# Optimization experiments

Measured on AMD Instinct MI355X. Metric: run time of the kernel, lower is better.

Reference implementation:

```python
import jax, jax.numpy as jnp
import numpy as np


def setup_inputs() -> dict:
    key = jax.random.key(0)
    ks = jax.random.split(key, 9)
    B, S, D = 4, 1024, 1024
    std = 0.02
    return {
        "x": jax.random.normal(ks[0], (B, S, D), dtype=jnp.float32),
        "W_q": jax.random.normal(ks[1], (D, D), dtype=jnp.float32) * std,
        "b_q": jnp.zeros((D,), dtype=jnp.float32),
        "W_k": jax.random.normal(ks[2], (D, D), dtype=jnp.float32) * std,
        "b_k": jnp.zeros((D,), dtype=jnp.float32),
        "W_v": jax.random.normal(ks[3], (D, D), dtype=jnp.float32) * std,
        "b_v": jnp.zeros((D,), dtype=jnp.float32),
        "W_o": jax.random.normal(ks[4], (D, D), dtype=jnp.float32) * std,
        "b_o": jnp.zeros((D,), dtype=jnp.float32),
        "n_heads": 16,
    }


def reference(x, W_q, b_q, W_k, b_k, W_v, b_v, W_o, b_o, n_heads):
    # x: [B, S, D]; torch Linear convention: y = x @ W.T + b, W is [out, in]
    B, S, D = x.shape
    d_k = D // n_heads
    scale = 1.0 / jnp.sqrt(jnp.asarray(d_k, dtype=x.dtype))

    def split_heads(t):  # [B,S,D] -> [B,H,S,d_k]
        return t.reshape(B, S, n_heads, d_k).transpose(0, 2, 1, 3)

    q = split_heads(x @ W_q.T + b_q)
    k = split_heads(x @ W_k.T + b_k)
    v = split_heads(x @ W_v.T + b_v)

    # scores: [B,H,L,S]
    scores = jnp.einsum("bhld,bhsd->bhls", q, k) * scale
    # causal bias (is_casual=True): -inf above the diagonal
    causal = jnp.tril(jnp.ones((S, S), dtype=bool))
    scores = jnp.where(causal[None, None, :, :], scores, jnp.asarray(-jnp.inf, dtype=scores.dtype))
    attn_w = jax.nn.softmax(scores, axis=-1)  # dropout_p = 0.0 -> identity

    y = jnp.einsum("bhls,bhsd->bhld", attn_w, v)  # [B,H,S,d_k]
    y = y.transpose(0, 2, 1, 3).reshape(B, S, D)
    y = y @ W_o.T + b_o  # output dropout p = 0.0 -> identity
    return (attn_w, y)
```

## Files before the change

kernel.cpp:

```cpp
#include <hip/hip_runtime.h>
#include <hip/hip_bf16.h>
#include <stdint.h>


typedef short short8 __attribute__((ext_vector_type(8)));
typedef short short4v __attribute__((ext_vector_type(4)));
typedef float f32x4 __attribute__((ext_vector_type(4)));

__device__ __forceinline__ short f2bf(float f) {
    union { __hip_bfloat16 h; short s; } u;
    u.h = __float2bfloat16(f);
    return u.s;
}
__device__ __forceinline__ float bf2f(short s) {
    union { uint32_t u; float f; } c;
    c.u = ((uint32_t)(uint16_t)s) << 16;
    return c.f;
}

#define GLD16(g, l) __builtin_amdgcn_global_load_lds( \
    (const __attribute__((address_space(1))) void*)(g), \
    (__attribute__((address_space(3))) void*)(l), 16, 0, 0)

__global__ __launch_bounds__(256) void castall_kernel(const float* __restrict__ x,
                                                      const float* __restrict__ w0,
                                                      const float* __restrict__ w1,
                                                      const float* __restrict__ w2,
                                                      const float* __restrict__ w3,
                                                      short* __restrict__ xb,
                                                      short* __restrict__ qkv,
                                                      short* __restrict__ wo) {
    const int seg = blockIdx.y;
    const float* src;
    short* dst;
    if (seg < 4) {
        src = seg == 0 ? w0 : seg == 1 ? w1 : seg == 2 ? w2 : w3;
        dst = seg < 3 ? qkv + (size_t)seg * 1048576 : wo;
    } else {
        src = x + (size_t)(seg - 4) * 1048576;
        dst = xb + (size_t)(seg - 4) * 1048576;
    }
    for (int i = blockIdx.x * 256 + threadIdx.x; i < 262144; i += gridDim.x * 256) {
        float4 v = ((const float4*)src)[i];
        short4v o;
        o[0] = f2bf(v.x); o[1] = f2bf(v.y); o[2] = f2bf(v.z); o[3] = f2bf(v.w);
        ((short4v*)dst)[i] = o;
    }
}

__global__ __launch_bounds__(256) void gemm_bt(const short* __restrict__ A,
                                               const short* __restrict__ Bw,
                                               const float* __restrict__ b0,
                                               const float* __restrict__ b1,
                                               const float* __restrict__ b2,
                                               short* __restrict__ outq,
                                               short* __restrict__ outk,
                                               short* __restrict__ outv,
                                               float* __restrict__ fout,
                                               int mode) {
    __shared__ __align__(16) short As[2][128 * 32];
    __shared__ __align__(16) short Bs[2][128 * 32];

    const int tid = threadIdx.x;
    const int wave = tid >> 6, lane = tid & 63;
    const int l15 = lane & 15, l4 = lane >> 4;
    const int wm = wave >> 1, wn = wave & 1;
    const int tM = blockIdx.y * 128, tN = blockIdx.x * 128;

    f32x4 acc[4][4] = {};

    auto stage = [&](int buf, int kt) {
        #pragma unroll
        for (int rep = 0; rep < 2; ++rep) {
            int slot = (wave * 2 + rep) * 64 + lane;
            int e0 = slot * 8;
            int row = e0 >> 5, col = e0 & 31;
            GLD16(&A[(size_t)(tM + row) * 1024 + kt + col],
                  (char*)&As[buf][0] + (size_t)(wave * 2 + rep) * 1024);
            GLD16(&Bw[(size_t)(tN + row) * 1024 + kt + col],
                  (char*)&Bs[buf][0] + (size_t)(wave * 2 + rep) * 1024);
        }
    };

    stage(0, 0);
    __syncthreads();
    int cur = 0;

    for (int t = 0; t < 32; ++t) {
        if (t < 31) stage(cur ^ 1, (t + 1) * 32);

        short8 af[4], bfr[4];
        #pragma unroll
        for (int f = 0; f < 4; ++f) {
            af[f]  = *(const short8*)&As[cur][(wm * 64 + f * 16 + l15) * 32 + l4 * 8];
            bfr[f] = *(const short8*)&Bs[cur][(wn * 64 + f * 16 + l15) * 32 + l4 * 8];
        }
        #pragma unroll
        for (int i = 0; i < 4; ++i)
            #pragma unroll
            for (int j = 0; j < 4; ++j)
                acc[i][j] = __builtin_amdgcn_mfma_f32_16x16x32_bf16(af[i], bfr[j], acc[i][j], 0, 0, 0);

        __syncthreads();
        cur ^= 1;
    }

    const int seg = tN >> 10;
    const float* bias = (mode == 3) ? b0 : (seg == 0 ? b0 : seg == 1 ? b1 : b2);

    #pragma unroll
    for (int i = 0; i < 4; ++i) {
        #pragma unroll
        for (int j = 0; j < 4; ++j) {
            if (mode == 4 && seg == 2) {
                int gr0 = tM + wm * 64 + i * 16 + l4 * 4;
                int gc  = tN + wn * 64 + j * 16 + l15;
                int nloc = gc & 1023;
                int bb = gr0 >> 10, s0 = gr0 & 1023, h = nloc >> 6, dk = nloc & 63;
                float bv_ = bias[nloc];
                short4v pk;
                #pragma unroll
                for (int v = 0; v < 4; ++v) pk[v] = f2bf(acc[i][j][v] + bv_);
                *(short4v*)&outv[(((size_t)bb * 16 + h) * 64 + dk) * 1024 + s0] = pk;
            } else {
                #pragma unroll
                for (int v = 0; v < 4; ++v) {
                    int gr = tM + wm * 64 + i * 16 + l4 * 4 + v;
                    int gc = tN + wn * 64 + j * 16 + l15;
                    if (mode == 3) {
                        fout[(size_t)gr * 1024 + gc] = acc[i][j][v] + bias[gc];
                    } else {
                        int nloc = gc & 1023;
                        float val = acc[i][j][v] + bias[nloc];
                        int bb = gr >> 10, s = gr & 1023, h = nloc >> 6, dk = nloc & 63;
                        if (seg == 0) {
                            outq[(((size_t)bb * 16 + h) * 1024 + s) * 64 + dk] = f2bf(val * 0.125f);
                        } else {
                            outk[(((size_t)bb * 16 + h) * 1024 + s) * 64 + dk] = f2bf(val);
                        }
                    }
                }
            }
        }
    }
}

__global__ __launch_bounds__(512, 4) void attn_kernel(const short* __restrict__ q,
                                                      const short* __restrict__ k,
                                                      const short* __restrict__ vT,
                                                      float* __restrict__ attn,
                                                      short* __restrict__ yh) {
    const int bh = blockIdx.x;
    const int y = blockIdx.y;
    const int qb = (y & 1) ? (31 - (y >> 1)) : (y >> 1);
    const int tid = threadIdx.x;
    const int wave = tid >> 6, lane = tid & 63;
    const int l15 = lane & 15, l4 = lane >> 4;
    const int rg = wave & 1, cg = wave >> 1;
    const int q0 = qb * 32;
    const int rbase = q0 + rg * 16;
    const int c0w = cg * 256;

    __shared__ __align__(16) short pb[32][1032];
    __shared__ float mred[4][32];
    __shared__ float sred[4][32];

    short8 qf[2];
    {
        const short* qrow = q + ((size_t)bh * 1024 + rbase + l15) * 64;
        qf[0] = *(const short8*)(qrow + l4 * 8);
        qf[1] = *(const short8*)(qrow + 32 + l4 * 8);
    }

    f32x4 sc[16] = {};
    #pragma unroll
    for (int cf = 0; cf < 16; ++cf) {
        if (c0w + cf * 16 < rbase + 16) {
            const short* krow = k + ((size_t)bh * 1024 + c0w + cf * 16 + l15) * 64;
            short8 kf0 = *(const short8*)(krow + l4 * 8);
            short8 kf1 = *(const short8*)(krow + 32 + l4 * 8);
            sc[cf] = __builtin_amdgcn_mfma_f32_16x16x32_bf16(qf[0], kf0, sc[cf], 0, 0, 0);
            sc[cf] = __builtin_amdgcn_mfma_f32_16x16x32_bf16(qf[1], kf1, sc[cf], 0, 0, 0);
        }
    }

    float mrow[4];
    #pragma unroll
    for (int j = 0; j < 4; ++j) {
        int rglob = rbase + l4 * 4 + j;
        float m = -1e30f;
        #pragma unroll
        for (int cf = 0; cf < 16; ++cf) {
            int col = c0w + cf * 16 + l15;
            m = fmaxf(m, (col <= rglob) ? sc[cf][j] : -1e30f);
        }
        m = fmaxf(m, __shfl_xor(m, 1));
        m = fmaxf(m, __shfl_xor(m, 2));
        m = fmaxf(m, __shfl_xor(m, 4));
        m = fmaxf(m, __shfl_xor(m, 8));
        mrow[j] = m;
    }
    if (l15 == 0) {
        #pragma unroll
        for (int j = 0; j < 4; ++j) mred[cg][rg * 16 + l4 * 4 + j] = mrow[j];
    }
    __syncthreads();
    #pragma unroll
    for (int j = 0; j < 4; ++j) {
        int r = rg * 16 + l4 * 4 + j;
        mrow[j] = fmaxf(fmaxf(mred[0][r], mred[1][r]), fmaxf(mred[2][r], mred[3][r]));
    }

    float inv[4], ls[4];
    #pragma unroll
    for (int j = 0; j < 4; ++j) {
        int rglob = rbase + l4 * 4 + j;
        float s = 0.f;
        #pragma unroll
        for (int cf = 0; cf < 16; ++cf) {
            int col = c0w + cf * 16 + l15;
            float e = (col <= rglob) ? __expf(sc[cf][j] - mrow[j]) : 0.f;
            sc[cf][j] = e;
            s += e;
        }
        s += __shfl_xor(s, 1);
        s += __shfl_xor(s, 2);
        s += __shfl_xor(s, 4);
        s += __shfl_xor(s, 8);
        ls[j] = s;
    }
    if (l15 == 0) {
        #pragma unroll
        for (int j = 0; j < 4; ++j) sred[cg][rg * 16 + l4 * 4 + j] = ls[j];
    }
    __syncthreads();
    #pragma unroll
    for (int j = 0; j < 4; ++j) {
        int r = rg * 16 + l4 * 4 + j;
        inv[j] = 1.0f / (sred[0][r] + sred[1][r] + sred[2][r] + sred[3][r]);
    }

    {
        float* abase = attn + (size_t)bh * 1048576;
        #pragma unroll
        for (int cf = 0; cf < 16; ++cf) {
            const bool keep = (c0w + cf * 16 < q0 + 64);
            const int col = c0w + cf * 16 + l15;
            #pragma unroll
            for (int j = 0; j < 4; ++j) {
                const int row = rg * 16 + l4 * 4 + j;
                float p = sc[cf][j] * inv[j];
                __builtin_nontemporal_store(p, &abase[(size_t)(q0 + row) * 1024 + col]);
                if (keep) pb[row][col] = f2bf(p);
            }
        }
    }
    __syncthreads();

    f32x4 yacc = {};
    {
        const short* vrow = vT + ((size_t)bh * 64 + cg * 16 + l15) * 1024;
        const int nch = (rbase + 16 + 31) >> 5;
        for (int ks = 0; ks < nch; ++ks) {
            short8 pf = *(const short8*)&pb[rg * 16 + l15][ks * 32 + l4 * 8];
            short8 vf = *(const short8*)(vrow + ks * 32 + l4 * 8);
            yacc = __builtin_amdgcn_mfma_f32_16x16x32_bf16(pf, vf, yacc, 0, 0, 0);
        }
    }

    const int b = bh >> 4, h = bh & 15;
    #pragma unroll
    for (int j = 0; j < 4; ++j) {
        yh[((size_t)b * 1024 + rbase + l4 * 4 + j) * 1024 + h * 64 + cg * 16 + l15] = f2bf(yacc[j]);
    }
}

extern "C" void kernel_launch(void* const* d_in, const int* in_sizes, int n_in,
                              void* d_out, int out_size, void* d_ws, size_t ws_size,
                              hipStream_t stream) {
    const float* x  = (const float*)d_in[0];
    const float* Wq = (const float*)d_in[1];
    const float* bq = (const float*)d_in[2];
    const float* Wk = (const float*)d_in[3];
    const float* bk = (const float*)d_in[4];
    const float* Wv = (const float*)d_in[5];
    const float* bv = (const float*)d_in[6];
    const float* Wo = (const float*)d_in[7];
    const float* bo = (const float*)d_in[8];

    char* ws = (char*)d_ws;
    short* xb   = (short*)(ws + ((size_t)0 << 20));
    short* wqkv = (short*)(ws + ((size_t)8 << 20));
    short* wob  = (short*)(ws + ((size_t)14 << 20));
    short* qbp  = (short*)(ws + ((size_t)16 << 20));
    short* kbp  = (short*)(ws + ((size_t)24 << 20));
    short* vTb  = (short*)(ws + ((size_t)32 << 20));
    short* yh   = (short*)(ws + ((size_t)40 << 20));

    float* attn = (float*)d_out;
    float* yout = attn + (size_t)67108864;

    castall_kernel<<<dim3(128, 8), 256, 0, stream>>>(x, Wq, Wk, Wv, Wo, xb, wqkv, wob);

    gemm_bt<<<dim3(24, 32), 256, 0, stream>>>(xb, wqkv, bq, bk, bv, qbp, kbp, vTb, nullptr, 4);

    attn_kernel<<<dim3(64, 32), 512, 0, stream>>>(qbp, kbp, vTb, attn, yh);

    gemm_bt<<<dim3(8, 32), 256, 0, stream>>>(yh, wob, bo, bo, bo, nullptr, nullptr, nullptr, yout, 3);
}
```

Baseline: 201.0 us.

## Use 256x256 tiles with block swizzle for the fused QKV projection GEMM

The shared mode-switched GEMM is split into two kernels. The QKV projection now uses 512-thread blocks computing 256x256 tiles (8 row fragments per wave), with a swizzled 1D block index to improve L2 reuse. The output projection keeps the original 128x128 kernel without the mode branches. Larger tiles raise arithmetic intensity per LDS load, but the launch shrinks to 192 blocks, fewer than the CU count, and register pressure grows.

After: 194.9 us. 3.1% less time.

```diff
diff --git a/kernel.cpp b/kernel.cpp
--- a/kernel.cpp
+++ b/kernel.cpp
@@ -48,26 +48,28 @@
     }
 }
 
-__global__ __launch_bounds__(256) void gemm_bt(const short* __restrict__ A,
-                                               const short* __restrict__ Bw,
-                                               const float* __restrict__ b0,
-                                               const float* __restrict__ b1,
-                                               const float* __restrict__ b2,
-                                               short* __restrict__ outq,
-                                               short* __restrict__ outk,
-                                               short* __restrict__ outv,
-                                               float* __restrict__ fout,
-                                               int mode) {
-    __shared__ __align__(16) short As[2][128 * 32];
-    __shared__ __align__(16) short Bs[2][128 * 32];
+__global__ __launch_bounds__(512, 2) void gemm_qkv256(const short* __restrict__ A,
+                                                      const short* __restrict__ Bw,
+                                                      const float* __restrict__ b0,
+                                                      const float* __restrict__ b1,
+                                                      const float* __restrict__ b2,
+                                                      short* __restrict__ outq,
+                                                      short* __restrict__ outk,
+                                                      short* __restrict__ outv) {
+    __shared__ __align__(16) short As[2][256 * 32];
+    __shared__ __align__(16) short Bs[2][256 * 32];
 
     const int tid = threadIdx.x;
     const int wave = tid >> 6, lane = tid & 63;
     const int l15 = lane & 15, l4 = lane >> 4;
-    const int wm = wave >> 1, wn = wave & 1;
-    const int tM = blockIdx.y * 128, tN = blockIdx.x * 128;
-
-    f32x4 acc[4][4] = {};
+    const int wm = wave >> 2, wn = wave & 3;
+
+    const int lin = blockIdx.x;
+    const int swz = (lin & 7) * 24 + (lin >> 3);
+    const int by = swz & 15, bx = swz >> 4;
+    const int tM = by * 256, tN = bx * 256;
+
+    f32x4 acc[8][4] = {};
 
     auto stage = [&](int buf, int kt) {
         #pragma unroll
@@ -89,14 +91,16 @@
     for (int t = 0; t < 32; ++t) {
         if (t < 31) stage(cur ^ 1, (t + 1) * 32);
 
-        short8 af[4], bfr[4];
-        #pragma unroll
-        for (int f = 0; f < 4; ++f) {
-            af[f]  = *(const short8*)&As[cur][(wm * 64 + f * 16 + l15) * 32 + l4 * 8];
+        short8 af[8], bfr[4];
+        #pragma unroll
+        for (int f = 0; f < 8; ++f)
+            af[f] = *(const short8*)&As[cur][(wm * 128 + f * 16 + l15) * 32 + l4 * 8];
+        #pragma unroll
+        for (int f = 0; f < 4; ++f)
             bfr[f] = *(const short8*)&Bs[cur][(wn * 64 + f * 16 + l15) * 32 + l4 * 8];
-        }
-        #pragma unroll
-        for (int i = 0; i < 4; ++i)
+
+        #pragma unroll
+        for (int i = 0; i < 8; ++i)
             #pragma unroll
             for (int j = 0; j < 4; ++j)
                 acc[i][j] = __builtin_amdgcn_mfma_f32_16x16x32_bf16(af[i], bfr[j], acc[i][j], 0, 0, 0);
@@ -106,18 +110,19 @@
     }
 
     const int seg = tN >> 10;
-    const float* bias = (mode == 3) ? b0 : (seg == 0 ? b0 : seg == 1 ? b1 : b2);
-
-    #pragma unroll
-    for (int i = 0; i < 4; ++i) {
+    const float* bias = seg == 0 ? b0 : seg == 1 ? b1 : b2;
+
+    #pragma unroll
+    for (int i = 0; i < 8; ++i) {
         #pragma unroll
         for (int j = 0; j < 4; ++j) {
-            if (mode == 4 && seg == 2) {
-                int gr0 = tM + wm * 64 + i * 16 + l4 * 4;
-                int gc  = tN + wn * 64 + j * 16 + l15;
-                int nloc = gc & 1023;
-                int bb = gr0 >> 10, s0 = gr0 & 1023, h = nloc >> 6, dk = nloc & 63;
-                float bv_ = bias[nloc];
+            int gc = tN + wn * 64 + j * 16 + l15;
+            int nloc = gc & 1023;
+            int h = nloc >> 6, dk = nloc & 63;
+            float bv_ = bias[nloc];
+            if (seg == 2) {
+                int gr0 = tM + wm * 128 + i * 16 + l4 * 4;
+                int bb = gr0 >> 10, s0 = gr0 & 1023;
                 short4v pk;
                 #pragma unroll
                 for (int v = 0; v < 4; ++v) pk[v] = f2bf(acc[i][j][v] + bv_);
@@ -125,21 +130,80 @@
             } else {
                 #pragma unroll
                 for (int v = 0; v < 4; ++v) {
-                    int gr = tM + wm * 64 + i * 16 + l4 * 4 + v;
-                    int gc = tN + wn * 64 + j * 16 + l15;
-                    if (mode == 3) {
-                        fout[(size_t)gr * 1024 + gc] = acc[i][j][v] + bias[gc];
+                    int gr = tM + wm * 128 + i * 16 + l4 * 4 + v;
+                    int bb = gr >> 10, s = gr & 1023;
+                    float val = acc[i][j][v] + bv_;
+                    if (seg == 0) {
+                        outq[(((size_t)bb * 16 + h) * 1024 + s) * 64 + dk] = f2bf(val * 0.125f);
                     } else {
-                        int nloc = gc & 1023;
-                        float val = acc[i][j][v] + bias[nloc];
-                        int bb = gr >> 10, s = gr & 1023, h = nloc >> 6, dk = nloc & 63;
-                        if (seg == 0) {
-                            outq[(((size_t)bb * 16 + h) * 1024 + s) * 64 + dk] = f2bf(val * 0.125f);
-                        } else {
-                            outk[(((size_t)bb * 16 + h) * 1024 + s) * 64 + dk] = f2bf(val);
-                        }
+                        outk[(((size_t)bb * 16 + h) * 1024 + s) * 64 + dk] = f2bf(val);
                     }
                 }
+            }
+        }
+    }
+}
+
+__global__ __launch_bounds__(256) void gemm_o(const short* __restrict__ A,
+                                              const short* __restrict__ Bw,
+                                              const float* __restrict__ bias,
+                                              float* __restrict__ fout) {
+    __shared__ __align__(16) short As[2][128 * 32];
+    __shared__ __align__(16) short Bs[2][128 * 32];
+
+    const int tid = threadIdx.x;
+    const int wave = tid >> 6, lane = tid & 63;
+    const int l15 = lane & 15, l4 = lane >> 4;
+    const int wm = wave >> 1, wn = wave & 1;
+    const int tM = blockIdx.y * 128, tN = blockIdx.x * 128;
+
+    f32x4 acc[4][4] = {};
+
+    auto stage = [&](int buf, int kt) {
+        #pragma unroll
+        for (int rep = 0; rep < 2; ++rep) {
+            int slot = (wave * 2 + rep) * 64 + lane;
+            int e0 = slot * 8;
+            int row = e0 >> 5, col = e0 & 31;
+            GLD16(&A[(size_t)(tM + row) * 1024 + kt + col],
+                  (char*)&As[buf][0] + (size_t)(wave * 2 + rep) * 1024);
+            GLD16(&Bw[(size_t)(tN + row) * 1024 + kt + col],
+                  (char*)&Bs[buf][0] + (size_t)(wave * 2 + rep) * 1024);
+        }
+    };
+
+    stage(0, 0);
+    __syncthreads();
+    int cur = 0;
+
+    for (int t = 0; t < 32; ++t) {
+        if (t < 31) stage(cur ^ 1, (t + 1) * 32);
+
+        short8 af[4], bfr[4];
+        #pragma unroll
+        for (int f = 0; f < 4; ++f) {
+            af[f]  = *(const short8*)&As[cur][(wm * 64 + f * 16 + l15) * 32 + l4 * 8];
+            bfr[f] = *(const short8*)&Bs[cur][(wn * 64 + f * 16 + l15) * 32 + l4 * 8];
+        }
+        #pragma unroll
+        for (int i = 0; i < 4; ++i)
+            #pragma unroll
+            for (int j = 0; j < 4; ++j)
+                acc[i][j] = __builtin_amdgcn_mfma_f32_16x16x32_bf16(af[i], bfr[j], acc[i][j], 0, 0, 0);
+
+        __syncthreads();
+        cur ^= 1;
+    }
+
+    #pragma unroll
+    for (int i = 0; i < 4; ++i) {
+        #pragma unroll
+        for (int j = 0; j < 4; ++j) {
+            #pragma unroll
+            for (int v = 0; v < 4; ++v) {
+                int gr = tM + wm * 64 + i * 16 + l4 * 4 + v;
+                int gc = tN + wn * 64 + j * 16 + l15;
+                fout[(size_t)gr * 1024 + gc] = acc[i][j][v] + bias[gc];
             }
         }
     }
@@ -302,9 +366,9 @@
 
     castall_kernel<<<dim3(128, 8), 256, 0, stream>>>(x, Wq, Wk, Wv, Wo, xb, wqkv, wob);
 
-    gemm_bt<<<dim3(24, 32), 256, 0, stream>>>(xb, wqkv, bq, bk, bv, qbp, kbp, vTb, nullptr, 4);
+    gemm_qkv256<<<192, 512, 0, stream>>>(xb, wqkv, bq, bk, bv, qbp, kbp, vTb);
 
     attn_kernel<<<dim3(64, 32), 512, 0, stream>>>(qbp, kbp, vTb, attn, yh);
 
-    gemm_bt<<<dim3(8, 32), 256, 0, stream>>>(yh, wob, bo, bo, bo, nullptr, nullptr, nullptr, yout, 3);
-}
+    gemm_o<<<dim3(8, 32), 256, 0, stream>>>(yh, wob, bo, yout);
+}
```
